# Optimization experiments

Hardware: AMD Instinct MI355X
Metric: run time of the kernel (lower is better)

Reference implementation:

```python
import jax, jax.numpy as jnp
import numpy as np

N = 100000          # nodes
E = 600000          # edges
H = 128             # hidden_dim
CF_DIM = 15         # input_dim - 1
NOISE_DIM = 32
NUM_CLASS = 6       # GraphConstructor.number_of_class
B = 64              # number of graphs in batch
BC = B * NUM_CLASS  # total clusters
LAYER_NUM = 3
NEG_SLOPE = 0.01


def setup_inputs() -> dict:
    key = jax.random.key(0)
    ks = jax.random.split(key, 12)
    cf = jax.random.normal(ks[0], (N, CF_DIM), jnp.float32)
    slf = jax.random.uniform(ks[1], (N,), jnp.float32)
    z = jax.random.normal(ks[2], (N, NOISE_DIM), jnp.float32)
    tr = jax.random.uniform(ks[3], (BC,), jnp.float32)
    W_enc = jax.random.normal(ks[4], (CF_DIM + 1 + NOISE_DIM, H), jnp.float32) * 0.05
    b_enc = jax.random.normal(ks[5], (H,), jnp.float32) * 0.05
    W_m = jax.random.normal(ks[6], (2 * H, H), jnp.float32) * 0.05
    b_m = jax.random.normal(ks[7], (H,), jnp.float32) * 0.05
    W_u = jax.random.normal(ks[8], (3 * H, H), jnp.float32) * 0.05
    b_u = jax.random.normal(ks[9], (H,), jnp.float32) * 0.05
    e = jax.random.randint(ks[10], (2, E), 0, N, jnp.int64)
    cc = jax.random.randint(ks[11], (N,), 0, BC, jnp.int64)
    cfb = cc // NUM_CLASS  # batch index consistent with global cluster index
    return {"cf": cf, "slf": slf, "z": z, "tr": tr,
            "W_enc": W_enc, "b_enc": b_enc, "W_m": W_m, "b_m": b_m,
            "W_u": W_u, "b_u": b_u, "e": e, "cc": cc, "cfb": cfb}


def _segment_mean(x, idx, num_segments):
    s = jax.ops.segment_sum(x, idx, num_segments=num_segments)
    c = jax.ops.segment_sum(jnp.ones((x.shape[0],), x.dtype), idx, num_segments=num_segments)
    return s / jnp.maximum(c, 1.0)[:, None]


def reference(cf, slf, z, tr, W_enc, b_enc, W_m, b_m, W_u, b_u, e, cc, cfb):
    # encoder: x = enc(cat(cf, slf, z))  (Linear, no activation since act='')
    x = jnp.concatenate([cf, slf[:, None], z], axis=-1) @ W_enc + b_enc  # [N, H]
    src, dst = e[0], e[1]  # PyG: x_j = x[src], x_i = x[dst], aggregate at dst
    for _ in range(LAYER_NUM):
        # message: MLP(cat(feature_i, feature_j)) per edge, mean-aggregated at dst
        msg = jnp.concatenate([x[dst], x[src]], axis=-1) @ W_m + b_m  # [E, H]
        aggr = _segment_mean(msg, dst, N)                              # [N, H]
        # cluster avg_pool scaled by target ratio, broadcast back to nodes
        pooled = _segment_mean(x, cc, BC) * tr[:, None]                # [BC, H]
        node_pool = pooled[cc]                                         # [N, H]
        upd = jnp.concatenate([x, aggr, node_pool], axis=-1) @ W_u + b_u
        upd = jnp.where(upd > 0, upd, NEG_SLOPE * upd)                 # LeakyReLU
        x = x + upd                                                    # residual
    return x
```

## Files before the change

### kernel.cpp

```cpp
#include <hip/hip_runtime.h>
#include <hip/hip_bf16.h>

#define N_NODES 100000
#define N_EDGES 600000
#define HD 128
#define NBC 384
#define SCAN_B 98
#define MAXFIX 4096
#define T32 ((N_NODES + 31) / 32)
#define GRID_F 1024
#define AGG_B (N_NODES / 4)
#define CAPB 16384

typedef __attribute__((ext_vector_type(8))) short s8v;
typedef __attribute__((ext_vector_type(4))) short s4v;
typedef __attribute__((ext_vector_type(4))) float f4v;
typedef __hip_bfloat16 bf16;

static __device__ __forceinline__ float bf2f(bf16 v) { return __bfloat162float(v); }
static __device__ __forceinline__ bf16 f2bf(float v) { return __float2bfloat16(v); }
static __device__ __forceinline__ float sh2f(short s) { bf16 h = *(bf16*)&s; return bf2f(h); }
static __device__ __forceinline__ short f2sh(float v) { bf16 h = f2bf(v); return *(short*)&h; }
static __device__ __forceinline__ float ldraw(const void* p, int i, int fp32) {
    return fp32 ? ((const float*)p)[i] : bf2f(((const bf16*)p)[i]);
}

static __device__ __forceinline__ void gl2lds16(const void* g, void* l) {
    __builtin_amdgcn_global_load_lds(
        (const __attribute__((address_space(1))) void*)g,
        (__attribute__((address_space(3))) void*)l, 16, 0, 0);
}

__global__ void k_init(const unsigned short* __restrict__ wraw, const int* __restrict__ eraw,
                       int* __restrict__ flags, int* __restrict__ ccount,
                       int* __restrict__ n0cnt, int* __restrict__ bcur) {
    int b = blockIdx.x, t = threadIdx.x;
    if (b == 0) {
        if (t < 64) {
            int bad = 0;
            for (int k = 0; k < 16; k++) {
                unsigned int u = ((unsigned int)wraw[t * 16 + k]) << 16;
                float f = fabsf(__uint_as_float(u));
                if (!(f <= 1e4f)) bad = 1;
            }
            unsigned long long m = __ballot(bad);
            if (t == 0) {
                flags[0] = m ? 1 : 0;
                flags[1] = (eraw[1] == 0 && eraw[3] == 0 && eraw[5] == 0 && eraw[7] == 0) ? 1 : 0;
            }
        }
    } else {
        if (t < 96) ((int4*)ccount)[t] = make_int4(0, 0, 0, 0);
        if (t == 96) *n0cnt = 0;
        if (t >= 128 && t < 128 + SCAN_B) bcur[t - 128] = 0;
    }
}

#define F_EDGE 586
#define F_XIN  (F_EDGE + 391)
#define F_CC   (F_XIN + 98)
#define F_WU   (F_CC + 192)
#define F_WM   (F_WU + 128)
#define F_WET  (F_WM + 32)
#define F_BC   (F_WET + 1)
#define F_TR   (F_BC + 2)
__global__ void k_ffront(const int* __restrict__ flags,
                         const void* cf_r, const void* slf_r, const void* z_r,
                         const void* tr_r, const void* Wenc_r, const void* benc_r,
                         const void* Wm_r, const void* bm_r, const void* Wu_r,
                         const void* bu_r, const int* __restrict__ e_r,
                         const int* __restrict__ cc_r,
                         bf16* __restrict__ xin, bf16* __restrict__ trc,
                         bf16* __restrict__ Wuc, bf16* __restrict__ Wmc,
                         bf16* __restrict__ buc, int* __restrict__ ccc,
                         int* __restrict__ ccount,
                         bf16* __restrict__ Wet, float* __restrict__ bc,
                         float* __restrict__ bcenc,
                         int* __restrict__ bcur, int* __restrict__ ebuf) {
    __shared__ short scfs[3840];
    __shared__ int hist[SCAN_B], hbase[SCAN_B], lcur[SCAN_B];
    __shared__ int ch[NBC];
    int b = blockIdx.x, t = threadIdx.x;
    int fp32 = flags[0];
    if (b < F_EDGE) {
        int i64f = flags[1];
        int e0 = b * 1024;
        if (t < SCAN_B) { hist[t] = 0; lcur[t] = 0; }
        __syncthreads();
        int sv[4], dv[4], bk[4];
#pragma unroll
        for (int k = 0; k < 4; k++) {
            int i = e0 + k * 256 + t;
            if (i < N_EDGES) {
                sv[k] = i64f ? e_r[2 * i] : e_r[i];
                dv[k] = i64f ? e_r[2 * (N_EDGES + i)] : e_r[N_EDGES + i];
                bk[k] = dv[k] >> 10;
                atomicAdd(&hist[bk[k]], 1);
            } else bk[k] = -1;
        }
        __syncthreads();
        if (t < SCAN_B && hist[t] > 0) hbase[t] = atomicAdd(&bcur[t], hist[t]);
        __syncthreads();
#pragma unroll
        for (int k = 0; k < 4; k++) {
            if (bk[k] >= 0) {
                int rel = hbase[bk[k]] + atomicAdd(&lcur[bk[k]], 1);
                if (rel < CAPB) ebuf[bk[k] * CAPB + rel] = (sv[k] << 10) | (dv[k] & 1023);
            }
        }
    } else if (b < F_XIN) {
        int bb = b - F_EDGE;
        int base = bb * 256;
        int cnt = min(3840, 1500000 - base * 15);
        if (fp32) {
            const float* cfp = (const float*)cf_r + (size_t)base * 15;
            f4v c0, c1, c2, c3;
            int e0 = t * 4, e1 = (256 + t) * 4, e2 = (512 + t) * 4, e3 = (768 + t) * 4;
            if (e0 < cnt) c0 = *(const f4v*)(cfp + e0);
            if (e1 < cnt) c1 = *(const f4v*)(cfp + e1);
            if (e2 < cnt) c2 = *(const f4v*)(cfp + e2);
            if (e3 < cnt) c3 = *(const f4v*)(cfp + e3);
            if (e0 < cnt) { for (int j = 0; j < 4; j++) scfs[e0 + j] = f2sh(c0[j]); }
            if (e1 < cnt) { for (int j = 0; j < 4; j++) scfs[e1 + j] = f2sh(c1[j]); }
            if (e2 < cnt) { for (int j = 0; j < 4; j++) scfs[e2 + j] = f2sh(c2[j]); }
            if (e3 < cnt) { for (int j = 0; j < 4; j++) scfs[e3 + j] = f2sh(c3[j]); }
        } else {
            const short* cfp = (const short*)cf_r + (size_t)base * 15;
            s8v c0, c1;
            int e0 = t * 8, e1 = (256 + t) * 8;
            if (e0 < cnt) c0 = *(const s8v*)(cfp + e0);
            if (e1 < cnt) c1 = *(const s8v*)(cfp + e1);
            if (e0 < cnt) *(s8v*)(scfs + e0) = c0;
            if (e1 < cnt) *(s8v*)(scfs + e1) = c1;
        }
        __syncthreads();
        int node = base + t;
        if (node >= N_NODES) return;
        short* xr = (short*)xin + (size_t)node * 64;
        const short* c = scfs + t * 15;
        s8v o0, o1;
#pragma unroll
        for (int r = 0; r < 8; r++) o0[r] = c[r];
#pragma unroll
        for (int r = 0; r < 7; r++) o1[r] = c[8 + r];
        o1[7] = fp32 ? f2sh(((const float*)slf_r)[node]) : ((const short*)slf_r)[node];
        if (fp32) {
            const float* zp = (const float*)z_r + (size_t)node * 32;
            f4v z0 = *(const f4v*)(zp +  0), z1 = *(const f4v*)(zp +  4);
            f4v z2 = *(const f4v*)(zp +  8), z3 = *(const f4v*)(zp + 12);
            f4v z4 = *(const f4v*)(zp + 16), z5 = *(const f4v*)(zp + 20);
            f4v z6 = *(const f4v*)(zp + 24), z7 = *(const f4v*)(zp + 28);
            s8v w0, w1, w2, w3;
#pragma unroll
            for (int r = 0; r < 4; r++) {
                w0[r] = f2sh(z0[r]); w0[4 + r] = f2sh(z1[r]);
                w1[r] = f2sh(z2[r]); w1[4 + r] = f2sh(z3[r]);
                w2[r] = f2sh(z4[r]); w2[4 + r] = f2sh(z5[r]);
                w3[r] = f2sh(z6[r]); w3[4 + r] = f2sh(z7[r]);
            }
            *(s8v*)(xr) = o0; *(s8v*)(xr + 8) = o1;
            *(s8v*)(xr + 16) = w0; *(s8v*)(xr + 24) = w1;
            *(s8v*)(xr + 32) = w2; *(s8v*)(xr + 40) = w3;
        } else {
            const short* zp = (const short*)z_r + (size_t)node * 32;
            s8v w0 = *(const s8v*)(zp), w1 = *(const s8v*)(zp + 8);
            s8v w2 = *(const s8v*)(zp + 16), w3 = *(const s8v*)(zp + 24);
            *(s8v*)(xr) = o0; *(s8v*)(xr + 8) = o1;
            *(s8v*)(xr + 16) = w0; *(s8v*)(xr + 24) = w1;
            *(s8v*)(xr + 32) = w2; *(s8v*)(xr + 40) = w3;
        }
        s8v zz = {0, 0, 0, 0, 0, 0, 0, 0};
        *(s8v*)(xr + 48) = zz;
        *(s8v*)(xr + 56) = zz;
    } else if (b < F_CC) {
        int i64f = flags[1];
        int nbase = (b - F_XIN) << 10;
        int nlim = min(1024, N_NODES - nbase);
        for (int j = t; j < NBC; j += 256) ch[j] = 0;
        __syncthreads();
#pragma unroll
        for (int k = 0; k < 4; k++) {
            int li = k * 256 + t;
            if (li < nlim) {
                int i = nbase + li;
                int v = i64f ? cc_r[2 * i] : cc_r[i];
                ccc[i] = v;
                atomicAdd(&ch[v], 1);
            }
        }
        __syncthreads();
        for (int j = t; j < NBC; j += 256) {
            int c = ch[j];
            if (c) atomicAdd(&ccount[j], c);
        }
    } else if (b < F_WU) {
        int i = (b - F_CC) * 256 + t;
        Wuc[i] = f2bf(ldraw(Wu_r, i, fp32));
    } else if (b < F_WM) {
        int i = (b - F_WU) * 256 + t;
        Wmc[i] = f2bf(ldraw(Wm_r, i, fp32));
    } else if (b < F_WET) {
        int i = (b - F_WM) * 256 + t;
        int w = i >> 6, kk = i & 63;
        float v = (kk < 48) ? ldraw(Wenc_r, kk * 128 + w, fp32) : 0.f;
        Wet[i] = f2bf(v);
    } else if (b < F_BC) {
        if (t < 128) {
            float acc = ldraw(bu_r, t, fp32);
#pragma unroll 4
            for (int j = 0; j < 128; j++)
                acc += ldraw(bm_r, j, fp32) * ldraw(Wu_r, (128 + j) * 128 + t, fp32);
            bc[t] = acc;
        } else {
            bcenc[t - 128] = ldraw(benc_r, t - 128, fp32);
            buc[t - 128] = f2bf(ldraw(bu_r, t - 128, fp32));
        }
    } else {
        int i = (b - F_BC) * 256 + t;
        if (i < 384) trc[i] = f2bf(ldraw(tr_r, i, fp32));
    }
}

__global__ void k_scan2(const int* __restrict__ bcur, int* __restrict__ bbase,
                        const int* __restrict__ ccount, int* __restrict__ coff,
                        int* __restrict__ ccur, int* __restrict__ rowptr) {
    __shared__ int sd[1024];
    int t = threadIdx.x;
    if (blockIdx.x == 0) {
        int v = (t < SCAN_B) ? bcur[t] : 0;
        sd[t] = v;
        __syncthreads();
#pragma unroll
        for (int off = 1; off < 128; off <<= 1) {
            int u = (t >= off) ? sd[t - off] : 0;
            __syncthreads();
            sd[t] += u;
            __syncthreads();
        }
        if (t < SCAN_B) bbase[t] = sd[t] - v;
        if (t == 0) rowptr[N_NODES] = N_EDGES;
    } else {
        int v = (t < NBC) ? ccount[t] : 0;
        sd[t] = v;
        __syncthreads();
#pragma unroll
        for (int off = 1; off < 512; off <<= 1) {
            int u = (t >= off) ? sd[t - off] : 0;
            __syncthreads();
            sd[t] += u;
            __syncthreads();
        }
        if (t < NBC) {
            int ex = sd[t] - v;
            coff[t] = ex;
            ccur[t] = ex;
            if (t == NBC - 1) coff[NBC] = sd[t];
        }
    }
}

#define M_W  6
#define M_PC (M_W + SCAN_B)
#define M_CF (M_PC + SCAN_B)
__global__ void k_mid(const bf16* __restrict__ Wmc, const bf16* __restrict__ Wuc,
                      bf16* __restrict__ Wc,
                      const int* __restrict__ ccc, int* __restrict__ ccur,
                      int* __restrict__ cnodes,
                      const int* __restrict__ bcur, const int* __restrict__ bbase,
                      const int* __restrict__ ebuf,
                      int* __restrict__ rowptr, int* __restrict__ deg,
                      int* __restrict__ colx,
                      int* __restrict__ n0list, int* __restrict__ n0cnt) {
    __shared__ short wm[4][2048];
    __shared__ int h2[1024], sd[1024];
    __shared__ int h[NBC], cb[NBC];
    int b = blockIdx.x, t = threadIdx.x;
    if (b < M_W) {
        int kw = b;
        int sub = t >> 8, lt = t & 255;
        int bp = kw * 4 + sub;
        int w = lt & 127, g = lt >> 7;
        int kk0 = bp * 16 + g * 8;
        if (kk0 >= 256) {
            s8v ov;
#pragma unroll
            for (int n = 0; n < 8; n++)
                ov[n] = *((const short*)Wuc + (kk0 + n) * 128 + w);
            *(s8v*)((short*)Wc + w * 384 + kk0) = ov;
            return;
        }
        *(s8v*)(wm[sub] + lt * 8) = *(const s8v*)((const short*)Wmc + bp * 2048 + lt * 8);
        __syncthreads();
        float acc[8];
#pragma unroll
        for (int n = 0; n < 8; n++) acc[n] = 0.f;
        const short* wup = (const short*)Wuc + 128 * 128 + w;
        const short* wmb = wm[sub] + (g * 8) * 128;
#pragma unroll 4
        for (int j = 0; j < 128; j++) {
            float wu = sh2f(wup[j * 128]);
#pragma unroll
            for (int n = 0; n < 8; n++)
                acc[n] += sh2f(wmb[n * 128 + j]) * wu;
        }
        s8v ov;
#pragma unroll
        for (int n = 0; n < 8; n++) {
            int kk = kk0 + n;
            float base = (kk < 128) ? sh2f(*((const short*)Wuc + kk * 128 + w)) : 0.f;
            ov[n] = f2sh(acc[n] + base);
        }
        *(s8v*)((short*)Wc + w * 384 + kk0) = ov;
    } else if (b < M_PC) {
        int bb = b - M_W;
        int nbase = bb << 10;
        int nlim = min(1024, N_NODES - nbase);
        int cnt = min(bcur[bb], CAPB);
        int base = bbase[bb];
        h2[t] = 0;
        __syncthreads();
        const int* eb = ebuf + bb * CAPB;
        for (int e = t; e < cnt; e += 1024) atomicAdd(&h2[eb[e] & 1023], 1);
        __syncthreads();
        int myDeg = h2[t];
        sd[t] = myDeg;
        __syncthreads();
#pragma unroll
        for (int off = 1; off < 1024; off <<= 1) {
            int u = (t >= off) ? sd[t - off] : 0;
            __syncthreads();
            sd[t] += u;
            __syncthreads();
        }
        int ex = sd[t] - myDeg;
        if (t < nlim) {
            rowptr[nbase + t] = base + ex;
            deg[nbase + t] = myDeg;
            if (myDeg == 0) {
                int p = atomicAdd(n0cnt, 1);
                if (p < MAXFIX) n0list[p] = nbase + t;
            }
        }
        __syncthreads();
        h2[t] = ex;
        __syncthreads();
        for (int e = t; e < cnt; e += 1024) {
            int v = eb[e];
            int p = atomicAdd(&h2[v & 1023], 1);
            colx[base + p] = v >> 10;
        }
    } else {
        int base = (b - M_PC) << 10;
        int node = base + t;
        if (t < NBC) h[t] = 0;
        __syncthreads();
        int cls = (node < N_NODES) ? ccc[node] : -1;
        if (cls >= 0) atomicAdd(&h[cls], 1);
        __syncthreads();
        if (t < NBC) {
            cb[t] = h[t] ? atomicAdd(&ccur[t], h[t]) : 0;
            h[t] = 0;
        }
        __syncthreads();
        if (cls >= 0) {
            int p = cb[cls] + atomicAdd(&h[cls], 1);
            cnodes[p] = node;
        }
    }
}

__global__ void k_front(const bf16* __restrict__ xin, const bf16* __restrict__ Wet,
                        const float* __restrict__ bcenc, bf16* __restrict__ xb) {
    int tid = threadIdx.x;
    int r0 = blockIdx.x * 64;
    int wave = tid >> 6, lane = tid & 63, quad = lane >> 4, nidx = lane & 15;
    int colbase = wave * 32;

    int arow[4];
#pragma unroll
    for (int rt = 0; rt < 4; rt++) {
        int gr = r0 + rt * 16 + nidx;
        arow[rt] = (gr < N_NODES) ? gr : (N_NODES - 1);
    }
    f4v acc[4][2];
#pragma unroll
    for (int rt = 0; rt < 4; rt++)
#pragma unroll
        for (int ct = 0; ct < 2; ct++) acc[rt][ct] = (f4v){0.f, 0.f, 0.f, 0.f};

#pragma unroll
    for (int s = 0; s < 2; s++) {
        int k0 = s * 32;
        s8v bfrag[4];
#pragma unroll
        for (int rt = 0; rt < 4; rt++)
            bfrag[rt] = *(const s8v*)((const short*)xin + (size_t)arow[rt] * 64 + k0 + quad * 8);
#pragma unroll
        for (int ct = 0; ct < 2; ct++) {
            s8v wfr = *(const s8v*)((const short*)Wet + (colbase + ct * 16 + nidx) * 64 + k0 + quad * 8);
#pragma unroll
            for (int rt = 0; rt < 4; rt++)
                acc[rt][ct] = __builtin_amdgcn_mfma_f32_16x16x32_bf16(wfr, bfrag[rt], acc[rt][ct], 0, 0, 0);
        }
    }
#pragma unroll
    for (int rt = 0; rt < 4; rt++) {
        int gr = r0 + rt * 16 + nidx;
        if (gr < N_NODES) {
#pragma unroll
            for (int ct = 0; ct < 2; ct++) {
                int wc0 = colbase + ct * 16 + quad * 4;
                f4v bv = *(const f4v*)(bcenc + wc0);
                size_t idx = (size_t)gr * HD + wc0;
                s4v ob;
#pragma unroll
                for (int r = 0; r < 4; r++) ob[r] = f2sh(acc[rt][ct][r] + bv[r]);
                *(s4v*)((short*)xb + idx) = ob;
            }
        }
    }
}

__global__ void k_aggpool(const bf16* __restrict__ xb, const int* __restrict__ rowptr,
                          const int* __restrict__ colx, bf16* __restrict__ mb,
                          const int* __restrict__ coff, const int* __restrict__ cnodes,
                          const bf16* __restrict__ trc, bf16* __restrict__ pooled) {
    __shared__ float red[8][128];
    int tid = threadIdx.x;
    if (blockIdx.x < NBC) {
        int cl = blockIdx.x;
        int lo = coff[cl], hi = coff[cl + 1];
        int cnt = hi - lo;
        int slot = tid >> 5, cg = tid & 31;
        float a0 = 0.f, a1 = 0.f, a2 = 0.f, a3 = 0.f;
        for (int i = lo + slot; i < hi; i += 8) {
            int nd = cnodes[i];
            s4v v = *(const s4v*)((const short*)xb + (size_t)nd * HD + cg * 4);
            a0 += sh2f(v[0]); a1 += sh2f(v[1]); a2 += sh2f(v[2]); a3 += sh2f(v[3]);
        }
        red[slot][cg * 4 + 0] = a0;
        red[slot][cg * 4 + 1] = a1;
        red[slot][cg * 4 + 2] = a2;
        red[slot][cg * 4 + 3] = a3;
        __syncthreads();
        if (tid < 128) {
            float s = 0.f;
#pragma unroll
            for (int k = 0; k < 8; k++) s += red[k][tid];
            float v = s / (float)(cnt > 1 ? cnt : 1) * bf2f(trc[cl]);
            pooled[cl * HD + tid] = f2bf(v);
        }
        return;
    }
    int wave = tid >> 6, lane = tid & 63;
    int node = (blockIdx.x - NBC) * 4 + wave;
    if (node >= N_NODES) return;
    int half = lane >> 5;
    int l = lane & 31;
    int lo = rowptr[node], hi = rowptr[node + 1];
    float a0 = 0.f, a1 = 0.f, a2 = 0.f, a3 = 0.f;
    for (int j0 = lo + half; j0 < hi; j0 += 8) {
        int i1 = j0 + 2, i2 = j0 + 4, i3 = j0 + 6;
        int s0 = colx[j0];
        int s1 = colx[i1 < hi ? i1 : j0];
        int s2 = colx[i2 < hi ? i2 : j0];
        int s3 = colx[i3 < hi ? i3 : j0];
        float m1 = (i1 < hi) ? 1.f : 0.f;
        float m2 = (i2 < hi) ? 1.f : 0.f;
        float m3 = (i3 < hi) ? 1.f : 0.f;
        s4v v0 = *(const s4v*)((const short*)xb + (size_t)s0 * HD + l * 4);
        s4v v1 = *(const s4v*)((const short*)xb + (size_t)s1 * HD + l * 4);
        s4v v2 = *(const s4v*)((const short*)xb + (size_t)s2 * HD + l * 4);
        s4v v3 = *(const s4v*)((const short*)xb + (size_t)s3 * HD + l * 4);
        a0 += sh2f(v0[0]) + m1 * sh2f(v1[0]) + m2 * sh2f(v2[0]) + m3 * sh2f(v3[0]);
        a1 += sh2f(v0[1]) + m1 * sh2f(v1[1]) + m2 * sh2f(v2[1]) + m3 * sh2f(v3[1]);
        a2 += sh2f(v0[2]) + m1 * sh2f(v1[2]) + m2 * sh2f(v2[2]) + m3 * sh2f(v3[2]);
        a3 += sh2f(v0[3]) + m1 * sh2f(v1[3]) + m2 * sh2f(v2[3]) + m3 * sh2f(v3[3]);
    }
    a0 += __shfl_down(a0, 32);
    a1 += __shfl_down(a1, 32);
    a2 += __shfl_down(a2, 32);
    a3 += __shfl_down(a3, 32);
    if (half == 0) {
        int d = hi - lo;
        float inv = 1.0f / (float)(d > 1 ? d : 1);
        s4v o;
        o[0] = f2sh(a0 * inv); o[1] = f2sh(a1 * inv);
        o[2] = f2sh(a2 * inv); o[3] = f2sh(a3 * inv);
        *(s4v*)((short*)mb + (size_t)node * HD + l * 4) = o;
    }
}

__global__ __launch_bounds__(256, 2) void k_fused2(
    const bf16* __restrict__ xb, const bf16* __restrict__ mb, const bf16* __restrict__ pooled,
    const bf16* __restrict__ Wc, const float* __restrict__ bc,
    const int* __restrict__ cc, const int* __restrict__ deg,
    const bf16* __restrict__ Wuc, const bf16* __restrict__ buc,
    const int* __restrict__ n0list, const int* __restrict__ n0cnt,
    bf16* __restrict__ xbo, const int* __restrict__ flags,
    void* __restrict__ out, int last) {
    __shared__ short Lx[32 * 128];
    __shared__ short Lm[32 * 128];
    __shared__ short Lp[32 * 128];
    __shared__ float fxv[128];
    __shared__ float fpv[128];
    int tid = threadIdx.x;
    int wave = tid >> 6, lane = tid & 63, quad = lane >> 4, nidx = lane & 15;
    int colbase = wave * 32;
    int fp32out = flags[0];

    s8v wfr[12][2];
#pragma unroll
    for (int ct = 0; ct < 2; ct++) {
        int wcol = colbase + ((nidx >> 2) << 3) + ct * 4 + (nidx & 3);
        const short* wrow = (const short*)Wc + (size_t)wcol * 384 + quad * 8;
#pragma unroll
        for (int s = 0; s < 12; s++) wfr[s][ct] = *(const s8v*)(wrow + s * 32);
    }
    int cb2 = colbase + quad * 8;
    f4v bv0 = *(const f4v*)(bc + cb2);
    f4v bv1 = *(const f4v*)(bc + cb2 + 4);

    int srow = lane >> 4;
    int sc = lane & 15;

    for (int t = blockIdx.x; t < T32; t += GRID_F) {
        int r0 = t * 32;
#pragma unroll
        for (int ii = 0; ii < 2; ii++) {
            int i = wave * 2 + ii;
            int lr = i * 4 + srow;
            int gr = r0 + lr;
            int grc = (gr < N_NODES) ? gr : (N_NODES - 1);
            int gc = sc ^ (lr & 15);
            gl2lds16((const short*)xb + (size_t)grc * HD + gc * 8, (char*)Lx + i * 1024);
            gl2lds16((const short*)mb + (size_t)grc * HD + gc * 8, (char*)Lm + i * 1024);
            int ci = cc[grc];
            gl2lds16((const short*)pooled + (size_t)ci * HD + gc * 8, (char*)Lp + i * 1024);
        }
        __syncthreads();

        f4v acc[2][2];
#pragma unroll
        for (int rt = 0; rt < 2; rt++)
#pragma unroll
            for (int ct = 0; ct < 2; ct++) acc[rt][ct] = (f4v){0.f, 0.f, 0.f, 0.f};

#pragma unroll
        for (int s = 0; s < 12; s++) {
            const short* Ls = (s < 4) ? Lx : ((s < 8) ? Lm : Lp);
            int c = (s & 3) * 4 + quad;
            s8v bfrag[2];
#pragma unroll
            for (int rt = 0; rt < 2; rt++) {
                int row = rt * 16 + nidx;
                int slot = c ^ nidx;
                bfrag[rt] = *(const s8v*)(Ls + row * 128 + slot * 8);
            }
#pragma unroll
            for (int ct = 0; ct < 2; ct++)
#pragma unroll
                for (int rt = 0; rt < 2; rt++)
                    acc[rt][ct] = __builtin_amdgcn_mfma_f32_16x16x32_bf16(wfr[s][ct], bfrag[rt], acc[rt][ct], 0, 0, 0);
        }

#pragma unroll
        for (int rt = 0; rt < 2; rt++) {
            int gr = r0 + rt * 16 + nidx;
            if (gr < N_NODES && deg[gr] > 0) {
                int row = rt * 16 + nidx;
                int slot = ((colbase >> 3) + quad) ^ nidx;
                s8v xo = *(const s8v*)(Lx + row * 128 + slot * 8);
                size_t idx = (size_t)gr * HD + cb2;
                float nv[8];
#pragma unroll
                for (int r = 0; r < 4; r++) {
                    float v0 = acc[rt][0][r] + bv0[r];
                    v0 = (v0 > 0.f) ? v0 : 0.01f * v0;
                    nv[r] = sh2f(xo[r]) + v0;
                    float v1 = acc[rt][1][r] + bv1[r];
                    v1 = (v1 > 0.f) ? v1 : 0.01f * v1;
                    nv[4 + r] = sh2f(xo[4 + r]) + v1;
                }
                if (last) {
                    if (fp32out) {
                        f4v o0 = {nv[0], nv[1], nv[2], nv[3]};
                        f4v o1 = {nv[4], nv[5], nv[6], nv[7]};
                        *(f4v*)((float*)out + idx) = o0;
                        *(f4v*)((float*)out + idx + 4) = o1;
                    } else {
                        s8v ob;
#pragma unroll
                        for (int r = 0; r < 8; r++) ob[r] = f2sh(nv[r]);
                        *(s8v*)((short*)out + idx) = ob;
                    }
                } else {
                    s8v ob;
#pragma unroll
                    for (int r = 0; r < 8; r++) ob[r] = f2sh(nv[r]);
                    *(s8v*)((short*)xbo + idx) = ob;
                }
            }
        }
        __syncthreads();
    }

    int cnt0 = *n0cnt;
    if (cnt0 > MAXFIX) cnt0 = MAXFIX;
    for (int j = blockIdx.x; j < cnt0; j += gridDim.x) {
        int v = n0list[j];
        if (tid < 128) {
            fxv[tid] = bf2f(xb[(size_t)v * HD + tid]);
            fpv[tid] = bf2f(pooled[cc[v] * HD + tid]);
        }
        __syncthreads();
        if (tid < 128) {
            float acc = bf2f(buc[tid]);
            for (int k = 0; k < 128; k++)
                acc += fxv[k] * bf2f(Wuc[k * 128 + tid]) + fpv[k] * bf2f(Wuc[(256 + k) * 128 + tid]);
            float u = acc > 0.f ? acc : 0.01f * acc;
            size_t idx = (size_t)v * HD + tid;
            float nv = fxv[tid] + u;
            if (last) {
                if (fp32out) ((float*)out)[idx] = nv;
                else ((bf16*)out)[idx] = f2bf(nv);
            } else {
                xbo[idx] = f2bf(nv);
            }
        }
        __syncthreads();
    }
}

extern "C" void kernel_launch(void* const* d_in, const int* in_sizes, int n_in,
                              void* d_out, int out_size, void* d_ws, size_t ws_size,
                              hipStream_t stream) {
    const void* cf_r = d_in[0];
    const void* slf_r = d_in[1];
    const void* z_r = d_in[2];
    const void* tr_r = d_in[3];
    const void* Wenc_r = d_in[4];
    const void* benc_r = d_in[5];
    const void* Wm_r = d_in[6];
    const void* bm_r = d_in[7];
    const void* Wu_r = d_in[8];
    const void* bu_r = d_in[9];
    const int* e_r = (const int*)d_in[10];
    const int* cc_r = (const int*)d_in[11];

    char* w = (char*)d_ws;
    auto alloc = [&](size_t bytes) -> char* {
        char* p = w;
        w += (bytes + 63) & ~(size_t)63;
        return p;
    };
    bf16* xb0 = (bf16*)alloc((size_t)N_NODES * HD * 2);
    bf16* xb1 = (bf16*)alloc((size_t)N_NODES * HD * 2);
    bf16* mb = (bf16*)alloc((size_t)N_NODES * HD * 2);
    bf16* xin = (bf16*)alloc((size_t)N_NODES * 64 * 2);
    bf16* Wc = (bf16*)alloc(128 * 384 * 2);
    float* bc = (float*)alloc(128 * 4);
    bf16* Wet = (bf16*)alloc(128 * 64 * 2);
    float* bcenc = (float*)alloc(128 * 4);
    bf16* pooled = (bf16*)alloc(NBC * HD * 2);
    int* deg = (int*)alloc(N_NODES * 4);
    int* rowptr = (int*)alloc((N_NODES + 1) * 4);
    int* colx = (int*)alloc(N_EDGES * 4);
    int* ccount = (int*)alloc(NBC * 4);
    int* coff = (int*)alloc((NBC + 1) * 4);
    int* ccur = (int*)alloc(NBC * 4);
    int* cnodes = (int*)alloc(N_NODES * 4);
    int* flags = (int*)alloc(64);
    int* n0list = (int*)alloc(MAXFIX * 4);
    int* n0cnt = (int*)alloc(64);
    bf16* trc = (bf16*)alloc(384 * 2);
    bf16* Wuc = (bf16*)alloc(49152 * 2);
    bf16* Wmc = (bf16*)alloc(32768 * 2);
    bf16* buc = (bf16*)alloc(128 * 2);
    int* ccc = (int*)alloc(N_NODES * 4);
    int* bcur = (int*)alloc(SCAN_B * 4);
    int* bbase = (int*)alloc(SCAN_B * 4);
    int* ebuf = (int*)alloc((size_t)SCAN_B * CAPB * 4);

    k_init<<<2, 256, 0, stream>>>((const unsigned short*)Wenc_r, e_r, flags,
                                  ccount, n0cnt, bcur);
    k_ffront<<<F_TR, 256, 0, stream>>>(flags, cf_r, slf_r, z_r, tr_r, Wenc_r, benc_r,
                                       Wm_r, bm_r, Wu_r, bu_r, e_r, cc_r,
                                       xin, trc, Wuc, Wmc, buc, ccc, ccount,
                                       Wet, bc, bcenc, bcur, ebuf);
    k_scan2<<<2, 1024, 0, stream>>>(bcur, bbase, ccount, coff, ccur, rowptr);
    k_mid<<<M_CF, 1024, 0, stream>>>(Wmc, Wuc, Wc, ccc, ccur, cnodes,
                                     bcur, bbase, ebuf, rowptr, deg, colx,
                                     n0list, n0cnt);
    k_front<<<(N_NODES + 63) / 64, 256, 0, stream>>>(xin, Wet, bcenc, xb0);

    bf16* xbufs[2] = {xb0, xb1};
    for (int layer = 0; layer < 3; layer++) {
        bf16* xbi = xbufs[layer & 1];
        bf16* xbo = xbufs[(layer + 1) & 1];
        int last = (layer == 2);
        k_aggpool<<<AGG_B + NBC, 256, 0, stream>>>(xbi, rowptr, colx, mb,
                                                   coff, cnodes, trc, pooled);
        k_fused2<<<GRID_F, 256, 0, stream>>>(xbi, mb, pooled, Wc, bc, ccc, deg,
                                             Wuc, buc, n0list, n0cnt,
                                             xbo, flags, d_out, last);
    }
}
```

Measured before the change: 378.3 us.

## Shard edge bucket counters, fuse encoder into k_mid, widen pool loads

Each edge-bucket atomic counter is split into four sub-counters chosen by block index, so fewer blocks contend on the same global atomic, and the bucket buffers are split to match. The separate encoder GEMM kernel is merged into k_mid as extra blocks, removing one launch and letting it run alongside the CSR build. The cluster pooling loop now loads 8 bf16 values per thread across 16 slots. The per-sub-bucket capacity is reduced, so a skewed destination distribution could overflow a sub-bucket and silently drop edges.

```diff
diff --git a/kernel.cpp b/kernel.cpp
--- a/kernel.cpp
+++ b/kernel.cpp
@@ -10,7 +10,7 @@
 #define T32 ((N_NODES + 31) / 32)
 #define GRID_F 1024
 #define AGG_B (N_NODES / 4)
-#define CAPB 16384
+#define CAPB4 4096
 
 typedef __attribute__((ext_vector_type(8))) short s8v;
 typedef __attribute__((ext_vector_type(4))) short s4v;
@@ -52,7 +52,7 @@
     } else {
         if (t < 96) ((int4*)ccount)[t] = make_int4(0, 0, 0, 0);
         if (t == 96) *n0cnt = 0;
-        if (t >= 128 && t < 128 + SCAN_B) bcur[t - 128] = 0;
+        for (int j = t; j < 4 * SCAN_B; j += 256) bcur[j] = 0;
     }
 }
 
@@ -85,6 +85,7 @@
     if (b < F_EDGE) {
         int i64f = flags[1];
         int e0 = b * 1024;
+        int rg = b & 3;
         if (t < SCAN_B) { hist[t] = 0; lcur[t] = 0; }
         __syncthreads();
         int sv[4], dv[4], bk[4];
@@ -99,13 +100,13 @@
             } else bk[k] = -1;
         }
         __syncthreads();
-        if (t < SCAN_B && hist[t] > 0) hbase[t] = atomicAdd(&bcur[t], hist[t]);
+        if (t < SCAN_B && hist[t] > 0) hbase[t] = atomicAdd(&bcur[rg * SCAN_B + t], hist[t]);
         __syncthreads();
 #pragma unroll
         for (int k = 0; k < 4; k++) {
             if (bk[k] >= 0) {
                 int rel = hbase[bk[k]] + atomicAdd(&lcur[bk[k]], 1);
-                if (rel < CAPB) ebuf[bk[k] * CAPB + rel] = (sv[k] << 10) | (dv[k] & 1023);
+                if (rel < CAPB4) ebuf[(bk[k] * 4 + rg) * CAPB4 + rel] = (sv[k] << 10) | (dv[k] & 1023);
             }
         }
     } else if (b < F_XIN) {
@@ -227,7 +228,11 @@
     __shared__ int sd[1024];
     int t = threadIdx.x;
     if (blockIdx.x == 0) {
-        int v = (t < SCAN_B) ? bcur[t] : 0;
+        int v = 0;
+        if (t < SCAN_B) {
+            v = min(bcur[t], CAPB4) + min(bcur[SCAN_B + t], CAPB4)
+              + min(bcur[2 * SCAN_B + t], CAPB4) + min(bcur[3 * SCAN_B + t], CAPB4);
+        }
         sd[t] = v;
         __syncthreads();
 #pragma unroll
@@ -262,6 +267,7 @@
 #define M_W  6
 #define M_PC (M_W + SCAN_B)
 #define M_CF (M_PC + SCAN_B)
+#define M_EN (M_CF + 391)
 __global__ void k_mid(const bf16* __restrict__ Wmc, const bf16* __restrict__ Wuc,
                       bf16* __restrict__ Wc,
                       const int* __restrict__ ccc, int* __restrict__ ccur,
@@ -270,7 +276,9 @@
                       const int* __restrict__ ebuf,
                       int* __restrict__ rowptr, int* __restrict__ deg,
                       int* __restrict__ colx,
-                      int* __restrict__ n0list, int* __restrict__ n0cnt) {
+                      int* __restrict__ n0list, int* __restrict__ n0cnt,
+                      const bf16* __restrict__ xin, const bf16* __restrict__ Wet,
+                      const float* __restrict__ bcenc, bf16* __restrict__ xb) {
     __shared__ short wm[4][2048];
     __shared__ int h2[1024], sd[1024];
     __shared__ int h[NBC], cb[NBC];
@@ -315,12 +323,17 @@
         int bb = b - M_W;
         int nbase = bb << 10;
         int nlim = min(1024, N_NODES - nbase);
-        int cnt = min(bcur[bb], CAPB);
         int base = bbase[bb];
+        int cnts[4];
+#pragma unroll
+        for (int r = 0; r < 4; r++) cnts[r] = min(bcur[r * SCAN_B + bb], CAPB4);
         h2[t] = 0;
         __syncthreads();
-        const int* eb = ebuf + bb * CAPB;
-        for (int e = t; e < cnt; e += 1024) atomicAdd(&h2[eb[e] & 1023], 1);
+#pragma unroll
+        for (int r = 0; r < 4; r++) {
+            const int* eb = ebuf + (bb * 4 + r) * CAPB4;
+            for (int e = t; e < cnts[r]; e += 1024) atomicAdd(&h2[eb[e] & 1023], 1);
+        }
         __syncthreads();
         int myDeg = h2[t];
         sd[t] = myDeg;
@@ -344,12 +357,16 @@
         __syncthreads();
         h2[t] = ex;
         __syncthreads();
-        for (int e = t; e < cnt; e += 1024) {
-            int v = eb[e];
-            int p = atomicAdd(&h2[v & 1023], 1);
-            colx[base + p] = v >> 10;
-        }
-    } else {
+#pragma unroll
+        for (int r = 0; r < 4; r++) {
+            const int* eb = ebuf + (bb * 4 + r) * CAPB4;
+            for (int e = t; e < cnts[r]; e += 1024) {
+                int v = eb[e];
+                int p = atomicAdd(&h2[v & 1023], 1);
+                colx[base + p] = v >> 10;
+            }
+        }
+    } else if (b < M_CF) {
         int base = (b - M_PC) << 10;
         int node = base + t;
         if (t < NBC) h[t] = 0;
@@ -366,56 +383,53 @@
             int p = cb[cls] + atomicAdd(&h[cls], 1);
             cnodes[p] = node;
         }
-    }
-}
-
-__global__ void k_front(const bf16* __restrict__ xin, const bf16* __restrict__ Wet,
-                        const float* __restrict__ bcenc, bf16* __restrict__ xb) {
-    int tid = threadIdx.x;
-    int r0 = blockIdx.x * 64;
-    int wave = tid >> 6, lane = tid & 63, quad = lane >> 4, nidx = lane & 15;
-    int colbase = wave * 32;
-
-    int arow[4];
-#pragma unroll
-    for (int rt = 0; rt < 4; rt++) {
-        int gr = r0 + rt * 16 + nidx;
-        arow[rt] = (gr < N_NODES) ? gr : (N_NODES - 1);
-    }
-    f4v acc[4][2];
-#pragma unroll
-    for (int rt = 0; rt < 4; rt++)
-#pragma unroll
-        for (int ct = 0; ct < 2; ct++) acc[rt][ct] = (f4v){0.f, 0.f, 0.f, 0.f};
-
-#pragma unroll
-    for (int s = 0; s < 2; s++) {
-        int k0 = s * 32;
-        s8v bfrag[4];
+    } else {
+        int sub = t >> 8, lt = t & 255;
+        int tile = (b - M_CF) * 4 + sub;
+        if (tile >= 1563) return;
+        int r0 = tile * 64;
+        int wave = lt >> 6, lane = lt & 63, quad = lane >> 4, nidx = lane & 15;
+        int colbase = wave * 32;
+        int arow[4];
+#pragma unroll
+        for (int rt = 0; rt < 4; rt++) {
+            int gr = r0 + rt * 16 + nidx;
+            arow[rt] = (gr < N_NODES) ? gr : (N_NODES - 1);
+        }
+        f4v acc[4][2];
 #pragma unroll
         for (int rt = 0; rt < 4; rt++)
-            bfrag[rt] = *(const s8v*)((const short*)xin + (size_t)arow[rt] * 64 + k0 + quad * 8);
-#pragma unroll
-        for (int ct = 0; ct < 2; ct++) {
-            s8v wfr = *(const s8v*)((const short*)Wet + (colbase + ct * 16 + nidx) * 64 + k0 + quad * 8);
+#pragma unroll
+            for (int ct = 0; ct < 2; ct++) acc[rt][ct] = (f4v){0.f, 0.f, 0.f, 0.f};
+#pragma unroll
+        for (int s = 0; s < 2; s++) {
+            int k0 = s * 32;
+            s8v bfrag[4];
 #pragma unroll
             for (int rt = 0; rt < 4; rt++)
-                acc[rt][ct] = __builtin_amdgcn_mfma_f32_16x16x32_bf16(wfr, bfrag[rt], acc[rt][ct], 0, 0, 0);
-        }
-    }
-#pragma unroll
-    for (int rt = 0; rt < 4; rt++) {
-        int gr = r0 + rt * 16 + nidx;
-        if (gr < N_NODES) {
+                bfrag[rt] = *(const s8v*)((const short*)xin + (size_t)arow[rt] * 64 + k0 + quad * 8);
 #pragma unroll
             for (int ct = 0; ct < 2; ct++) {
-                int wc0 = colbase + ct * 16 + quad * 4;
-                f4v bv = *(const f4v*)(bcenc + wc0);
-                size_t idx = (size_t)gr * HD + wc0;
-                s4v ob;
-#pragma unroll
-                for (int r = 0; r < 4; r++) ob[r] = f2sh(acc[rt][ct][r] + bv[r]);
-                *(s4v*)((short*)xb + idx) = ob;
+                s8v wfr = *(const s8v*)((const short*)Wet + (colbase + ct * 16 + nidx) * 64 + k0 + quad * 8);
+#pragma unroll
+                for (int rt = 0; rt < 4; rt++)
+                    acc[rt][ct] = __builtin_amdgcn_mfma_f32_16x16x32_bf16(wfr, bfrag[rt], acc[rt][ct], 0, 0, 0);
+            }
+        }
+#pragma unroll
+        for (int rt = 0; rt < 4; rt++) {
+            int gr = r0 + rt * 16 + nidx;
+            if (gr < N_NODES) {
+#pragma unroll
+                for (int ct = 0; ct < 2; ct++) {
+                    int wc0 = colbase + ct * 16 + quad * 4;
+                    f4v bv = *(const f4v*)(bcenc + wc0);
+                    size_t idx = (size_t)gr * HD + wc0;
+                    s4v ob;
+#pragma unroll
+                    for (int r = 0; r < 4; r++) ob[r] = f2sh(acc[rt][ct][r] + bv[r]);
+                    *(s4v*)((short*)xb + idx) = ob;
+                }
             }
         }
     }
@@ -425,28 +439,29 @@
                           const int* __restrict__ colx, bf16* __restrict__ mb,
                           const int* __restrict__ coff, const int* __restrict__ cnodes,
                           const bf16* __restrict__ trc, bf16* __restrict__ pooled) {
-    __shared__ float red[8][128];
+    __shared__ float red[16][128];
     int tid = threadIdx.x;
     if (blockIdx.x < NBC) {
         int cl = blockIdx.x;
         int lo = coff[cl], hi = coff[cl + 1];
         int cnt = hi - lo;
-        int slot = tid >> 5, cg = tid & 31;
-        float a0 = 0.f, a1 = 0.f, a2 = 0.f, a3 = 0.f;
-        for (int i = lo + slot; i < hi; i += 8) {
+        int slot = tid >> 4, cg = tid & 15;
+        float a[8];
+#pragma unroll
+        for (int j = 0; j < 8; j++) a[j] = 0.f;
+        for (int i = lo + slot; i < hi; i += 16) {
             int nd = cnodes[i];
-            s4v v = *(const s4v*)((const short*)xb + (size_t)nd * HD + cg * 4);
-            a0 += sh2f(v[0]); a1 += sh2f(v[1]); a2 += sh2f(v[2]); a3 += sh2f(v[3]);
-        }
-        red[slot][cg * 4 + 0] = a0;
-        red[slot][cg * 4 + 1] = a1;
-        red[slot][cg * 4 + 2] = a2;
-        red[slot][cg * 4 + 3] = a3;
+            s8v v = *(const s8v*)((const short*)xb + (size_t)nd * HD + cg * 8);
+#pragma unroll
+            for (int j = 0; j < 8; j++) a[j] += sh2f(v[j]);
+        }
+#pragma unroll
+        for (int j = 0; j < 8; j++) red[slot][cg * 8 + j] = a[j];
         __syncthreads();
         if (tid < 128) {
             float s = 0.f;
 #pragma unroll
-            for (int k = 0; k < 8; k++) s += red[k][tid];
+            for (int k = 0; k < 16; k++) s += red[k][tid];
             float v = s / (float)(cnt > 1 ? cnt : 1) * bf2f(trc[cl]);
             pooled[cl * HD + tid] = f2bf(v);
         }
@@ -678,9 +693,9 @@
     bf16* Wmc = (bf16*)alloc(32768 * 2);
     bf16* buc = (bf16*)alloc(128 * 2);
     int* ccc = (int*)alloc(N_NODES * 4);
-    int* bcur = (int*)alloc(SCAN_B * 4);
+    int* bcur = (int*)alloc(4 * SCAN_B * 4);
     int* bbase = (int*)alloc(SCAN_B * 4);
-    int* ebuf = (int*)alloc((size_t)SCAN_B * CAPB * 4);
+    int* ebuf = (int*)alloc((size_t)SCAN_B * 4 * CAPB4 * 4);
 
     k_init<<<2, 256, 0, stream>>>((const unsigned short*)Wenc_r, e_r, flags,
                                   ccount, n0cnt, bcur);
@@ -689,10 +704,9 @@
                                        xin, trc, Wuc, Wmc, buc, ccc, ccount,
                                        Wet, bc, bcenc, bcur, ebuf);
     k_scan2<<<2, 1024, 0, stream>>>(bcur, bbase, ccount, coff, ccur, rowptr);
-    k_mid<<<M_CF, 1024, 0, stream>>>(Wmc, Wuc, Wc, ccc, ccur, cnodes,
+    k_mid<<<M_EN, 1024, 0, stream>>>(Wmc, Wuc, Wc, ccc, ccur, cnodes,
                                      bcur, bbase, ebuf, rowptr, deg, colx,
-                                     n0list, n0cnt);
-    k_front<<<(N_NODES + 63) / 64, 256, 0, stream>>>(xin, Wet, bcenc, xb0);
+                                     n0list, n0cnt, xin, Wet, bcenc, xb0);
 
     bf16* xbufs[2] = {xb0, xb1};
     for (int layer = 0; layer < 3; layer++) {
```

New measurement: 359.3 us, median of 2. -5.0%, faster.
